# Kernel tuning notes

Measured on AMD Instinct MI355X. Metric: run time of the kernel, lower is better.

The kernel has to match this reference:

```python
import jax, jax.numpy as jnp
import numpy as np

N_NODES = 10000
N_EDGES = 640000
IN_FEATS = 128
H_FEATS1 = 128
NUM_OUTPUTS = 64


def setup_inputs() -> dict:
    key = jax.random.key(0)
    k0, k1, k2, k3, k4 = jax.random.split(key, 5)
    in_feat = jax.random.normal(k0, (N_NODES, IN_FEATS), dtype=jnp.float32)
    src = jax.random.randint(k1, (N_EDGES,), 0, N_NODES, dtype=jnp.int64)
    dst = jax.random.randint(k2, (N_EDGES,), 0, N_NODES, dtype=jnp.int64)
    W1 = jax.random.normal(k3, (IN_FEATS, H_FEATS1), dtype=jnp.float32) * 0.05
    b1 = jnp.zeros((H_FEATS1,), dtype=jnp.float32)
    W2 = jax.random.normal(k4, (H_FEATS1, NUM_OUTPUTS), dtype=jnp.float32) * 0.05
    b2 = jnp.zeros((NUM_OUTPUTS,), dtype=jnp.float32)
    return {"in_feat": in_feat, "src": src, "dst": dst,
            "W1": W1, "b1": b1, "W2": W2, "b2": b2}


def _graph_conv(src, dst, x, W, b):
    # DGL GraphConv with norm='both': out = D_out^{-1/2} A^T-agg D_in^{-1/2} x W + b
    n = x.shape[0]
    ones = jnp.ones((src.shape[0],), dtype=x.dtype)
    deg_out = jnp.clip(jax.ops.segment_sum(ones, src, num_segments=n), 1.0)
    deg_in = jnp.clip(jax.ops.segment_sum(ones, dst, num_segments=n), 1.0)
    h = x * jax.lax.rsqrt(deg_out)[:, None]            # src-side normalization
    agg = jax.ops.segment_sum(h[src], dst, num_segments=n)  # SpMM: sum over in-edges
    agg = agg * jax.lax.rsqrt(deg_in)[:, None]         # dst-side normalization
    return agg @ W + b


def reference(in_feat, src, dst, W1, b1, W2, b2):
    h = _graph_conv(src, dst, in_feat, W1, b1)
    h = jax.nn.relu(h)  # dropout=0 -> identity
    return _graph_conv(src, dst, h, W2, b2)
```

## Files before the change

kernel.cpp:

```cpp
#include <hip/hip_runtime.h>
#include <hip/hip_fp16.h>

#define NFEAT 128
#define NOUT  64
#define PCAP  128
#define HB    256

__global__ void hist_kernel(const int* __restrict__ src, const int* __restrict__ dst,
                            unsigned short* __restrict__ hist_src,
                            unsigned short* __restrict__ hist_dst,
                            unsigned int* __restrict__ pe,
                            const float* __restrict__ x, uint4* __restrict__ xh,
                            int nN, int nE) {
    extern __shared__ int bins[];
    int b = blockIdx.x;
    int per = (nE + HB - 1) / HB;
    int lo = b * per, hi = min(lo + per, nE);
    for (int i = threadIdx.x; i < nN; i += blockDim.x) bins[i] = 0;
    __syncthreads();
    for (int e = lo + threadIdx.x; e < hi; e += blockDim.x) {
        int s = src[e], d = dst[e];
        atomicAdd(&bins[d], 1);
        atomicAdd(&bins[s], 0x10000);
        pe[e] = (unsigned int)(unsigned short)s | ((unsigned int)d << 16);
    }
    __syncthreads();
    for (int i = threadIdx.x; i < nN; i += blockDim.x) {
        int v = bins[i];
        hist_dst[(size_t)b * nN + i] = (unsigned short)(v & 0xFFFF);
        hist_src[(size_t)b * nN + i] = (unsigned short)(v >> 16);
    }
    const float4* xf = (const float4*)x;
    int nchunk = nN * NFEAT / 8;
    for (int c = blockIdx.x * blockDim.x + threadIdx.x; c < nchunk; c += gridDim.x * blockDim.x) {
        float4 a = xf[2 * c], bb = xf[2 * c + 1];
        __half2 h[4] = {__floats2half2_rn(a.x, a.y),  __floats2half2_rn(a.z, a.w),
                        __floats2half2_rn(bb.x, bb.y), __floats2half2_rn(bb.z, bb.w)};
        xh[c] = *(uint4*)h;
    }
}

__global__ void offsets_kernel(const unsigned short* __restrict__ hist_src,
                               const unsigned short* __restrict__ hist_dst,
                               unsigned short* __restrict__ base_rel,
                               unsigned short* __restrict__ deg_in,
                               float* __restrict__ rs_in, float* __restrict__ rs_out, int nN) {
    int tid = blockIdx.x * blockDim.x + threadIdx.x;
    if (tid < nN) {
        int i = tid;
        int run = 0;
#pragma unroll 16
        for (int b = 0; b < HB; b++) {
            base_rel[(size_t)b * nN + i] = (unsigned short)run;
            run += hist_dst[(size_t)b * nN + i];
        }
        deg_in[i] = (unsigned short)min(run, PCAP);
        rs_in[i] = rsqrtf(fmaxf((float)run, 1.0f));
    } else if (tid < 2 * nN) {
        int i = tid - nN;
        int to = 0;
#pragma unroll 16
        for (int b = 0; b < HB; b++) to += hist_src[(size_t)b * nN + i];
        rs_out[i] = rsqrtf(fmaxf((float)to, 1.0f));
    }
}

__global__ void scatter_kernel(const unsigned int* __restrict__ pe,
                               const unsigned short* __restrict__ base_rel,
                               unsigned short* __restrict__ csr, int nN, int nE) {
    extern __shared__ int cur[];
    int b = blockIdx.x;
    int per = (nE + HB - 1) / HB;
    int lo = b * per, hi = min(lo + per, nE);
    for (int i = threadIdx.x; i < nN; i += blockDim.x)
        cur[i] = base_rel[(size_t)b * nN + i];
    __syncthreads();
    for (int e = lo + threadIdx.x; e < hi; e += blockDim.x) {
        unsigned int v = pe[e];
        int s = v & 0xFFFF, d = v >> 16;
        int pos = atomicAdd(&cur[d], 1);
        if (pos < PCAP)
            csr[(size_t)d * PCAP + pos] = (unsigned short)s;
    }
}

__device__ __forceinline__ void fma8(float* acc, uint4 v, float f) {
    const __half2* h = (const __half2*)&v;
    float2 p0 = __half22float2(h[0]), p1 = __half22float2(h[1]);
    float2 p2 = __half22float2(h[2]), p3 = __half22float2(h[3]);
    acc[0] += p0.x * f; acc[1] += p0.y * f; acc[2] += p1.x * f; acc[3] += p1.y * f;
    acc[4] += p2.x * f; acc[5] += p2.y * f; acc[6] += p3.x * f; acc[7] += p3.y * f;
}

__global__ void gather1_kernel(const unsigned short* __restrict__ deg_in,
                               const unsigned short* __restrict__ csr,
                               const uint4* __restrict__ xh, const float* __restrict__ rs_out,
                               const float* __restrict__ rs_in,
                               float* __restrict__ t, int nN) {
    __shared__ unsigned short eids[4][PCAP];
    __shared__ float rsv[4][PCAP];
    int tid = threadIdx.x;
    int w = tid >> 6, lane = tid & 63;
    int i = blockIdx.x * 4 + w;
    int n = deg_in[i];
    ((unsigned int*)eids[w])[lane] = ((const unsigned int*)(csr + (size_t)i * PCAP))[lane];
    for (int e = lane; e < n; e += 64) rsv[w][e] = rs_out[eids[w][e]];

    int quad = lane >> 4;
    int g = lane & 15;
    float s_in = rs_in[i];
    float acc[8] = {0.f, 0.f, 0.f, 0.f, 0.f, 0.f, 0.f, 0.f};
    int e = quad;
    for (; e + 28 < n; e += 32) {
        uint4 vv[8]; float ff[8];
#pragma unroll
        for (int u = 0; u < 8; u++) {
            int s = eids[w][e + 4 * u];
            ff[u] = rsv[w][e + 4 * u];
            vv[u] = xh[(size_t)s * 16 + g];
        }
#pragma unroll
        for (int u = 0; u < 8; u++) fma8(acc, vv[u], ff[u]);
    }
    for (; e + 12 < n; e += 16) {
        uint4 vv[4]; float ff[4];
#pragma unroll
        for (int u = 0; u < 4; u++) {
            int s = eids[w][e + 4 * u];
            ff[u] = rsv[w][e + 4 * u];
            vv[u] = xh[(size_t)s * 16 + g];
        }
#pragma unroll
        for (int u = 0; u < 4; u++) fma8(acc, vv[u], ff[u]);
    }
    for (; e < n; e += 4) {
        fma8(acc, xh[(size_t)eids[w][e] * 16 + g], rsv[w][e]);
    }
#pragma unroll
    for (int d = 16; d <= 32; d <<= 1)
#pragma unroll
        for (int k = 0; k < 8; k++) acc[k] += __shfl_xor(acc[k], d);
    if (lane < 16) {
        float4 o0 = {acc[0] * s_in, acc[1] * s_in, acc[2] * s_in, acc[3] * s_in};
        float4 o1 = {acc[4] * s_in, acc[5] * s_in, acc[6] * s_in, acc[7] * s_in};
        float4* tp = (float4*)(t + (size_t)i * NFEAT + g * 8);
        tp[0] = o0; tp[1] = o1;
    }
}

#define NPB 16
__global__ void mlp_kernel(const float* __restrict__ t_in, const float* __restrict__ rs_out,
                           const float* __restrict__ W1, const float* __restrict__ b1,
                           const float* __restrict__ W2, __half* __restrict__ zh, int nN) {
    __shared__ float ts[NPB][NFEAT];
    __shared__ float h1[NPB][NFEAT];
    int i0 = blockIdx.x * NPB;
    int tid = threadIdx.x;
    for (int t2 = tid; t2 < NPB * NFEAT; t2 += 256)
        ts[t2 >> 7][t2 & 127] = t_in[(size_t)i0 * NFEAT + t2];
    __syncthreads();
    {
        int j = tid & 127;
        int g = (tid >> 7) * 8;
        float a[8];
        float b = b1[j];
#pragma unroll
        for (int u = 0; u < 8; u++) a[u] = b;
#pragma unroll 8
        for (int k = 0; k < NFEAT; k++) {
            float w = W1[k * NFEAT + j];
#pragma unroll
            for (int u = 0; u < 8; u++) a[u] += ts[g + u][k] * w;
        }
#pragma unroll
        for (int u = 0; u < 8; u++) h1[g + u][j] = fmaxf(a[u], 0.0f);
    }
    __syncthreads();
    {
        int j2 = tid & 63;
        int g2 = (tid >> 6) * 4;
        float c[4] = {0.f, 0.f, 0.f, 0.f};
#pragma unroll 8
        for (int k = 0; k < NFEAT; k++) {
            float w = W2[k * NOUT + j2];
#pragma unroll
            for (int u = 0; u < 4; u++) c[u] += h1[g2 + u][k] * w;
        }
#pragma unroll
        for (int u = 0; u < 4; u++)
            zh[(size_t)(i0 + g2 + u) * NOUT + j2] = __float2half_rn(c[u] * rs_out[i0 + g2 + u]);
    }
}

__global__ void gather2_kernel(const unsigned short* __restrict__ deg_in,
                               const unsigned short* __restrict__ csr,
                               const uint4* __restrict__ zh, const float* __restrict__ rs_in,
                               const float* __restrict__ b2, float* __restrict__ out, int nN) {
    __shared__ unsigned short eids[4][PCAP];
    int tid = threadIdx.x;
    int w = tid >> 6, lane = tid & 63;
    int i = blockIdx.x * 4 + w;
    int n = deg_in[i];
    ((unsigned int*)eids[w])[lane] = ((const unsigned int*)(csr + (size_t)i * PCAP))[lane];

    int oct = lane >> 3;
    int g = lane & 7;
    float acc[8] = {0.f, 0.f, 0.f, 0.f, 0.f, 0.f, 0.f, 0.f};
    int e = oct;
    for (; e + 56 < n; e += 64) {
        uint4 vv[8];
#pragma unroll
        for (int u = 0; u < 8; u++) vv[u] = zh[(size_t)eids[w][e + 8 * u] * 8 + g];
#pragma unroll
        for (int u = 0; u < 8; u++) fma8(acc, vv[u], 1.0f);
    }
    for (; e + 24 < n; e += 32) {
        uint4 vv[4];
#pragma unroll
        for (int u = 0; u < 4; u++) vv[u] = zh[(size_t)eids[w][e + 8 * u] * 8 + g];
#pragma unroll
        for (int u = 0; u < 4; u++) fma8(acc, vv[u], 1.0f);
    }
    for (; e < n; e += 8) {
        fma8(acc, zh[(size_t)eids[w][e] * 8 + g], 1.0f);
    }
#pragma unroll
    for (int d = 8; d <= 32; d <<= 1)
#pragma unroll
        for (int k = 0; k < 8; k++) acc[k] += __shfl_xor(acc[k], d);
    if (lane < 8) {
        float s = rs_in[i];
        float4 bb0 = ((const float4*)b2)[2 * g], bb1 = ((const float4*)b2)[2 * g + 1];
        float4 o0 = {acc[0] * s + bb0.x, acc[1] * s + bb0.y, acc[2] * s + bb0.z, acc[3] * s + bb0.w};
        float4 o1 = {acc[4] * s + bb1.x, acc[5] * s + bb1.y, acc[6] * s + bb1.z, acc[7] * s + bb1.w};
        float4* op = (float4*)(out + (size_t)i * NOUT + g * 8);
        op[0] = o0; op[1] = o1;
    }
}

extern "C" void kernel_launch(void* const* d_in, const int* in_sizes, int n_in,
                              void* d_out, int out_size, void* d_ws, size_t ws_size,
                              hipStream_t stream) {
    const float* x  = (const float*)d_in[0];
    const int* src  = (const int*)d_in[1];
    const int* dst  = (const int*)d_in[2];
    const float* W1 = (const float*)d_in[3];
    const float* b1 = (const float*)d_in[4];
    const float* W2 = (const float*)d_in[5];
    const float* b2 = (const float*)d_in[6];
    float* out = (float*)d_out;

    const int nN = in_sizes[0] / NFEAT;
    const int nE = in_sizes[1];

    char* p = (char*)d_ws;
    unsigned short* hist_src = (unsigned short*)p; p += (size_t)HB * nN * 2;
    unsigned short* hist_dst = (unsigned short*)p; p += (size_t)HB * nN * 2;
    unsigned short* base_rel = (unsigned short*)p; p += (size_t)HB * nN * 2;
    unsigned int*   pe       = (unsigned int*)p;   p += (size_t)nE * 4;
    unsigned short* csr      = (unsigned short*)p; p += (size_t)nN * PCAP * 2;
    unsigned short* deg_in   = (unsigned short*)p; p += (size_t)nN * 2;
    float* rs_in  = (float*)p; p += (size_t)nN * sizeof(float);
    float* rs_out = (float*)p; p += (size_t)nN * sizeof(float);
    uint4* xh = (uint4*)p; p += (size_t)nN * NFEAT * 2;
    float* t = (float*)p; p += (size_t)nN * NFEAT * sizeof(float);
    __half* zh = (__half*)p; p += (size_t)nN * NOUT * 2;

    hist_kernel<<<HB, 256, (size_t)nN * sizeof(int), stream>>>(
        src, dst, hist_src, hist_dst, pe, x, xh, nN, nE);
    offsets_kernel<<<(2 * nN + 255) / 256, 256, 0, stream>>>(
        hist_src, hist_dst, base_rel, deg_in, rs_in, rs_out, nN);
    scatter_kernel<<<HB, 256, (size_t)nN * sizeof(int), stream>>>(
        pe, base_rel, csr, nN, nE);
    gather1_kernel<<<nN / 4, 256, 0, stream>>>(deg_in, csr, xh, rs_out, rs_in, t, nN);
    mlp_kernel<<<nN / NPB, 256, 0, stream>>>(t, rs_out, W1, b1, W2, zh, nN);
    gather2_kernel<<<nN / 4, 256, 0, stream>>>(deg_in, csr, (const uint4*)zh, rs_in, b2, out, nN);
}
```

Before: 153.9 us.

## Fuse first-layer gather with MLP kernel to keep aggregates in shared memory

Merges the first SpMM gather and the two-layer dense MLP into one kernel: each block gathers 16 nodes (4 per wave, sequentially) into shared memory, then runs the W1/ReLU/W2 products directly. This removes the fp32 intermediate buffer write/read and one kernel launch. In exchange, the gather runs with 4x fewer blocks and extra block-wide barriers per node round, reducing latency hiding for the irregular loads.

```diff
diff --git a/kernel.cpp b/kernel.cpp
--- a/kernel.cpp
+++ b/kernel.cpp
@@ -5,6 +5,7 @@
 #define NOUT  64
 #define PCAP  128
 #define HB    256
+#define NPB   16
 
 __global__ void hist_kernel(const int* __restrict__ src, const int* __restrict__ dst,
                             unsigned short* __restrict__ hist_src,
@@ -92,88 +93,87 @@
     acc[4] += p2.x * f; acc[5] += p2.y * f; acc[6] += p3.x * f; acc[7] += p3.y * f;
 }
 
-__global__ void gather1_kernel(const unsigned short* __restrict__ deg_in,
-                               const unsigned short* __restrict__ csr,
-                               const uint4* __restrict__ xh, const float* __restrict__ rs_out,
-                               const float* __restrict__ rs_in,
-                               float* __restrict__ t, int nN) {
+__global__ void gather_mlp_kernel(const unsigned short* __restrict__ deg_in,
+                                  const unsigned short* __restrict__ csr,
+                                  const uint4* __restrict__ xh,
+                                  const float* __restrict__ rs_out,
+                                  const float* __restrict__ rs_in,
+                                  const float* __restrict__ W1, const float* __restrict__ b1,
+                                  const float* __restrict__ W2, __half* __restrict__ zh,
+                                  int nN) {
+    __shared__ float ts[NPB][NFEAT];
+    __shared__ float h1[NPB][NFEAT];
     __shared__ unsigned short eids[4][PCAP];
     __shared__ float rsv[4][PCAP];
     int tid = threadIdx.x;
     int w = tid >> 6, lane = tid & 63;
-    int i = blockIdx.x * 4 + w;
-    int n = deg_in[i];
-    ((unsigned int*)eids[w])[lane] = ((const unsigned int*)(csr + (size_t)i * PCAP))[lane];
-    for (int e = lane; e < n; e += 64) rsv[w][e] = rs_out[eids[w][e]];
-
+    int i0 = blockIdx.x * NPB;
     int quad = lane >> 4;
     int g = lane & 15;
-    float s_in = rs_in[i];
-    float acc[8] = {0.f, 0.f, 0.f, 0.f, 0.f, 0.f, 0.f, 0.f};
-    int e = quad;
-    for (; e + 28 < n; e += 32) {
-        uint4 vv[8]; float ff[8];
-#pragma unroll
-        for (int u = 0; u < 8; u++) {
-            int s = eids[w][e + 4 * u];
-            ff[u] = rsv[w][e + 4 * u];
-            vv[u] = xh[(size_t)s * 16 + g];
-        }
-#pragma unroll
-        for (int u = 0; u < 8; u++) fma8(acc, vv[u], ff[u]);
-    }
-    for (; e + 12 < n; e += 16) {
-        uint4 vv[4]; float ff[4];
-#pragma unroll
-        for (int u = 0; u < 4; u++) {
-            int s = eids[w][e + 4 * u];
-            ff[u] = rsv[w][e + 4 * u];
-            vv[u] = xh[(size_t)s * 16 + g];
-        }
-#pragma unroll
-        for (int u = 0; u < 4; u++) fma8(acc, vv[u], ff[u]);
-    }
-    for (; e < n; e += 4) {
-        fma8(acc, xh[(size_t)eids[w][e] * 16 + g], rsv[w][e]);
-    }
-#pragma unroll
-    for (int d = 16; d <= 32; d <<= 1)
-#pragma unroll
-        for (int k = 0; k < 8; k++) acc[k] += __shfl_xor(acc[k], d);
-    if (lane < 16) {
-        float4 o0 = {acc[0] * s_in, acc[1] * s_in, acc[2] * s_in, acc[3] * s_in};
-        float4 o1 = {acc[4] * s_in, acc[5] * s_in, acc[6] * s_in, acc[7] * s_in};
-        float4* tp = (float4*)(t + (size_t)i * NFEAT + g * 8);
-        tp[0] = o0; tp[1] = o1;
-    }
-}
-
-#define NPB 16
-__global__ void mlp_kernel(const float* __restrict__ t_in, const float* __restrict__ rs_out,
-                           const float* __restrict__ W1, const float* __restrict__ b1,
-                           const float* __restrict__ W2, __half* __restrict__ zh, int nN) {
-    __shared__ float ts[NPB][NFEAT];
-    __shared__ float h1[NPB][NFEAT];
-    int i0 = blockIdx.x * NPB;
-    int tid = threadIdx.x;
-    for (int t2 = tid; t2 < NPB * NFEAT; t2 += 256)
-        ts[t2 >> 7][t2 & 127] = t_in[(size_t)i0 * NFEAT + t2];
-    __syncthreads();
+
+    for (int r = 0; r < 4; r++) {
+        int node = w * 4 + r;
+        int i = i0 + node;
+        int n = deg_in[i];
+        ((unsigned int*)eids[w])[lane] =
+            ((const unsigned int*)(csr + (size_t)i * PCAP))[lane];
+        __syncthreads();
+        for (int e = lane; e < n; e += 64) rsv[w][e] = rs_out[eids[w][e]];
+        __syncthreads();
+        float s_in = rs_in[i];
+        float acc[8] = {0.f, 0.f, 0.f, 0.f, 0.f, 0.f, 0.f, 0.f};
+        int e = quad;
+        for (; e + 28 < n; e += 32) {
+            uint4 vv[8]; float ff[8];
+#pragma unroll
+            for (int u = 0; u < 8; u++) {
+                int s = eids[w][e + 4 * u];
+                ff[u] = rsv[w][e + 4 * u];
+                vv[u] = xh[(size_t)s * 16 + g];
+            }
+#pragma unroll
+            for (int u = 0; u < 8; u++) fma8(acc, vv[u], ff[u]);
+        }
+        for (; e + 12 < n; e += 16) {
+            uint4 vv[4]; float ff[4];
+#pragma unroll
+            for (int u = 0; u < 4; u++) {
+                int s = eids[w][e + 4 * u];
+                ff[u] = rsv[w][e + 4 * u];
+                vv[u] = xh[(size_t)s * 16 + g];
+            }
+#pragma unroll
+            for (int u = 0; u < 4; u++) fma8(acc, vv[u], ff[u]);
+        }
+        for (; e < n; e += 4)
+            fma8(acc, xh[(size_t)eids[w][e] * 16 + g], rsv[w][e]);
+#pragma unroll
+        for (int d = 16; d <= 32; d <<= 1)
+#pragma unroll
+            for (int k = 0; k < 8; k++) acc[k] += __shfl_xor(acc[k], d);
+        if (lane < 16) {
+            float4 o0 = {acc[0] * s_in, acc[1] * s_in, acc[2] * s_in, acc[3] * s_in};
+            float4 o1 = {acc[4] * s_in, acc[5] * s_in, acc[6] * s_in, acc[7] * s_in};
+            float4* tp = (float4*)(&ts[node][g * 8]);
+            tp[0] = o0; tp[1] = o1;
+        }
+        __syncthreads();
+    }
     {
         int j = tid & 127;
-        int g = (tid >> 7) * 8;
+        int gq = (tid >> 7) * 8;
         float a[8];
-        float b = b1[j];
-#pragma unroll
-        for (int u = 0; u < 8; u++) a[u] = b;
+        float bb = b1[j];
+#pragma unroll
+        for (int u = 0; u < 8; u++) a[u] = bb;
 #pragma unroll 8
         for (int k = 0; k < NFEAT; k++) {
-            float w = W1[k * NFEAT + j];
-#pragma unroll
-            for (int u = 0; u < 8; u++) a[u] += ts[g + u][k] * w;
-        }
-#pragma unroll
-        for (int u = 0; u < 8; u++) h1[g + u][j] = fmaxf(a[u], 0.0f);
+            float wv = W1[k * NFEAT + j];
+#pragma unroll
+            for (int u = 0; u < 8; u++) a[u] += ts[gq + u][k] * wv;
+        }
+#pragma unroll
+        for (int u = 0; u < 8; u++) h1[gq + u][j] = fmaxf(a[u], 0.0f);
     }
     __syncthreads();
     {
@@ -182,13 +182,14 @@
         float c[4] = {0.f, 0.f, 0.f, 0.f};
 #pragma unroll 8
         for (int k = 0; k < NFEAT; k++) {
-            float w = W2[k * NOUT + j2];
-#pragma unroll
-            for (int u = 0; u < 4; u++) c[u] += h1[g2 + u][k] * w;
+            float wv = W2[k * NOUT + j2];
+#pragma unroll
+            for (int u = 0; u < 4; u++) c[u] += h1[g2 + u][k] * wv;
         }
 #pragma unroll
         for (int u = 0; u < 4; u++)
-            zh[(size_t)(i0 + g2 + u) * NOUT + j2] = __float2half_rn(c[u] * rs_out[i0 + g2 + u]);
+            zh[(size_t)(i0 + g2 + u) * NOUT + j2] =
+                __float2half_rn(c[u] * rs_out[i0 + g2 + u]);
     }
 }
 
@@ -221,9 +222,8 @@
 #pragma unroll
         for (int u = 0; u < 4; u++) fma8(acc, vv[u], 1.0f);
     }
-    for (; e < n; e += 8) {
+    for (; e < n; e += 8)
         fma8(acc, zh[(size_t)eids[w][e] * 8 + g], 1.0f);
-    }
 #pragma unroll
     for (int d = 8; d <= 32; d <<= 1)
 #pragma unroll
@@ -265,6 +265,7 @@
     uint4* xh = (uint4*)p; p += (size_t)nN * NFEAT * 2;
     float* t = (float*)p; p += (size_t)nN * NFEAT * sizeof(float);
     __half* zh = (__half*)p; p += (size_t)nN * NOUT * 2;
+    (void)t;
 
     hist_kernel<<<HB, 256, (size_t)nN * sizeof(int), stream>>>(
         src, dst, hist_src, hist_dst, pe, x, xh, nN, nE);
@@ -272,7 +273,8 @@
         hist_src, hist_dst, base_rel, deg_in, rs_in, rs_out, nN);
     scatter_kernel<<<HB, 256, (size_t)nN * sizeof(int), stream>>>(
         pe, base_rel, csr, nN, nE);
-    gather1_kernel<<<nN / 4, 256, 0, stream>>>(deg_in, csr, xh, rs_out, rs_in, t, nN);
-    mlp_kernel<<<nN / NPB, 256, 0, stream>>>(t, rs_out, W1, b1, W2, zh, nN);
-    gather2_kernel<<<nN / 4, 256, 0, stream>>>(deg_in, csr, (const uint4*)zh, rs_in, b2, out, nN);
-}
+    gather_mlp_kernel<<<nN / NPB, 256, 0, stream>>>(
+        deg_in, csr, xh, rs_out, rs_in, W1, b1, W2, zh, nN);
+    gather2_kernel<<<nN / 4, 256, 0, stream>>>(
+        deg_in, csr, (const uint4*)zh, rs_in, b2, out, nN);
+}
```

Result: no change. 154.3 us (+0.2%).
